# Optimization experiments

Measured on AMD Instinct MI355X. Metric: run time of the kernel, lower is better.

The kernel has to match this reference:

```python
import jax, jax.numpy as jnp
from jax import lax
import numpy as np

B, T, D, H, K = 16, 2048, 512, 512, 2

def setup_inputs() -> dict:
    key = jax.random.key(0)
    k1, k2, k3 = jax.random.split(key, 3)
    inputs = jax.random.normal(k1, (B, T, D), dtype=jnp.float32)
    conv_w = jax.random.normal(k2, (3 * H, D, K), dtype=jnp.float32) * (1.0 / np.sqrt(D * K))
    conv_b = jax.random.normal(k3, (3 * H,), dtype=jnp.float32) * 0.01
    return {"inputs": inputs, "conv_w": conv_w, "conv_b": conv_b}

def reference(inputs, conv_w, conv_b):
    # inputs: [B, T, D]; conv_w: [3H, D, K]; causal conv via left-pad K-1
    k = conv_w.shape[-1]
    h = conv_w.shape[0] // 3
    x = jnp.transpose(inputs, (0, 2, 1))                      # [B, D, T]
    x = jnp.pad(x, ((0, 0), (0, 0), (k - 1, 0)))              # left pad
    gates = lax.conv_general_dilated(
        x, conv_w, window_strides=(1,), padding='VALID',
        dimension_numbers=('NCH', 'OIH', 'NCH'))              # [B, 3H, T]
    gates = jnp.transpose(gates, (0, 2, 1)) + conv_b          # [B, T, 3H]
    Z, F, O = jnp.split(gates, 3, axis=2)
    Z = jnp.tanh(Z)
    F = jax.nn.sigmoid(F)
    O = jax.nn.sigmoid(O)

    # fo-pool: c_t = f_t * c_{t-1} + (1 - f_t) * z_t, c_{-1} = 0
    def step(c, zf):
        z, f = zf
        c_ = f * c + (1.0 - f) * z
        return c_, c_

    c0 = jnp.zeros((Z.shape[0], h), dtype=Z.dtype)
    _, C = lax.scan(step, c0, (jnp.swapaxes(Z, 0, 1), jnp.swapaxes(F, 0, 1)))
    C = jnp.swapaxes(C, 0, 1)                                 # [B, T, H]
    return C, O * C
```

## Files before the change

kernel.cpp:

```cpp
#include <hip/hip_runtime.h>


#define MTOT 32768
#define NTOT 1536
#define KTOT 1024
#define DCH  512
#define TLEN 2048
#define NB   16

#define LC2    32
#define NCH    64
#define CHAINS 8192

typedef __bf16 bf16x8 __attribute__((ext_vector_type(8)));
typedef float  f32x4  __attribute__((ext_vector_type(4)));

__device__ __forceinline__ unsigned short f2bf(float x) {
    unsigned u = __float_as_uint(x);
    u += 0x7FFFu + ((u >> 16) & 1u);
    return (unsigned short)(u >> 16);
}
__device__ __forceinline__ float bf2f(unsigned short h) {
    return __uint_as_float(((unsigned)h) << 16);
}
__device__ __forceinline__ float sigmoidf_(float x) {
    return 1.f / (1.f + __expf(-x));
}

__global__ __launch_bounds__(256) void make_A(const float* __restrict__ in,
                                              unsigned short* __restrict__ A) {
    size_t i = (size_t)blockIdx.x * 256 + threadIdx.x;
    size_t e = i * 8;
    size_t m = e >> 10;
    int    j = (int)(e & 1023);
    alignas(16) unsigned short h[8];
    if (((m & (TLEN - 1)) == 0) && (j < DCH)) {
#pragma unroll
        for (int r = 0; r < 8; ++r) h[r] = 0;
    } else {
        const float* src = in + ((long long)m - 1) * DCH + j;
        float4 a = *(const float4*)src;
        float4 b = *(const float4*)(src + 4);
        h[0] = f2bf(a.x); h[1] = f2bf(a.y); h[2] = f2bf(a.z); h[3] = f2bf(a.w);
        h[4] = f2bf(b.x); h[5] = f2bf(b.y); h[6] = f2bf(b.z); h[7] = f2bf(b.w);
    }
    *(int4*)(A + e) = *(const int4*)h;
}

__global__ __launch_bounds__(256) void make_B(const float* __restrict__ w,
                                              unsigned short* __restrict__ Bt) {
    int i = blockIdx.x * 256 + threadIdx.x;
    int o = i >> 9, d = i & 511;
    float w0 = w[(size_t)(o * 512 + d) * 2];
    float w1 = w[(size_t)(o * 512 + d) * 2 + 1];
    Bt[(size_t)o * 1024 + d]       = f2bf(w0);
    Bt[(size_t)o * 1024 + 512 + d] = f2bf(w1);
}

__global__ __launch_bounds__(512) void gemm_gates(const unsigned short* __restrict__ A,
                                                  const unsigned short* __restrict__ B,
                                                  const float* __restrict__ bias,
                                                  unsigned short* __restrict__ GT) {
    __shared__ int4 lds4[8192];

    const int tid = threadIdx.x;
    const int bx0 = blockIdx.x;
    const int bx  = (bx0 & 7) * 96 + (bx0 >> 3);
    const int mT  = bx / 6, nT = bx % 6;
    const int m0  = mT * 256, n0 = nT * 256;

    const int sq = (tid & 3) ^ ((tid >> 3) & 3);
    const unsigned short* ga = A + (size_t)(m0 + (tid >> 2)) * 1024 + sq * 8;
    const unsigned short* gb = B + (size_t)(n0 + (tid >> 2)) * 1024 + sq * 8;
    char* ldsc = (char*)lds4;

    const int lane = tid & 63;
    const int wv   = tid >> 6;
    const int wm   = wv >> 2, wn = wv & 3;
    const int lr   = lane & 15, lq = lane >> 4;

    int aoff[2][4], boff[4];
#pragma unroll
    for (int ih = 0; ih < 2; ++ih)
#pragma unroll
        for (int i = 0; i < 4; ++i) {
            int r = wm * 128 + ih * 64 + i * 16 + lr;
            aoff[ih][i] = r * 4 + (lq ^ ((r >> 1) & 3));
        }
#pragma unroll
    for (int j = 0; j < 4; ++j) {
        int c = wn * 64 + j * 16 + lr;
        boff[j] = 1024 + c * 4 + (lq ^ ((c >> 1) & 3));
    }

    f32x4 acc[8][4] = {};
    bf16x8 bfr[4];

#define GLL(SRC, DOFF) __builtin_amdgcn_global_load_lds( \
        (__attribute__((address_space(1))) void*)(void*)(SRC), \
        (__attribute__((address_space(3))) void*)(ldsc + (DOFF)), 16, 0, 0)

#define STG_A(S, KH) { const size_t go_ = (size_t)(S) * 64 + (size_t)(KH) * 32; \
        const int db_ = ((((S) & 1) * 4096 + (KH) * 2048) * 16) + tid * 16; \
        GLL(ga + go_, db_); GLL(ga + 131072 + go_, db_ + 8192); }
#define STG_B(S, KH) { const size_t go_ = (size_t)(S) * 64 + (size_t)(KH) * 32; \
        const int db_ = ((((S) & 1) * 4096 + (KH) * 2048) * 16) + 16384 + tid * 16; \
        GLL(gb + go_, db_); GLL(gb + 131072 + go_, db_ + 8192); }

#define VMW(N) asm volatile("s_waitcnt vmcnt(" #N ")" ::: "memory")

#define PHASE(D, KH, IH, RDB, STG, VM) { \
        const int rg_ = (D) * 4096 + (KH) * 2048; \
        if (RDB) { \
            _Pragma("unroll") \
            for (int j = 0; j < 4; ++j) bfr[j] = __builtin_bit_cast(bf16x8, lds4[rg_ + boff[j]]); \
        } \
        bf16x8 af_[4]; \
        _Pragma("unroll") \
        for (int i = 0; i < 4; ++i) af_[i] = __builtin_bit_cast(bf16x8, lds4[rg_ + aoff[IH][i]]); \
        STG; \
        __builtin_amdgcn_sched_barrier(0); \
        __builtin_amdgcn_s_barrier(); \
        __builtin_amdgcn_sched_barrier(0); \
        __builtin_amdgcn_s_setprio(1); \
        _Pragma("unroll") \
        for (int i = 0; i < 4; ++i) \
            _Pragma("unroll") \
            for (int j = 0; j < 4; ++j) \
                acc[(IH) * 4 + i][j] = __builtin_amdgcn_mfma_f32_16x16x32_bf16( \
                    af_[i], bfr[j], acc[(IH) * 4 + i][j], 0, 0, 0); \
        __builtin_amdgcn_s_setprio(0); \
        VM; \
        __builtin_amdgcn_sched_barrier(0); \
        __builtin_amdgcn_s_barrier(); \
        __builtin_amdgcn_sched_barrier(0); \
    }

    STG_A(0, 0); STG_B(0, 0); STG_A(0, 1); STG_B(0, 1); STG_A(1, 0); STG_B(1, 0);
    VMW(8);
    __builtin_amdgcn_s_barrier();
    __builtin_amdgcn_sched_barrier(0);

    for (int t = 0; t < 14; t += 2) {
        PHASE(0, 0, 0, 1, STG_A(t + 1, 1), ((void)0));
        PHASE(0, 0, 1, 0, STG_B(t + 1, 1), VMW(8));
        PHASE(0, 1, 0, 1, STG_A(t + 2, 0), ((void)0));
        PHASE(0, 1, 1, 0, STG_B(t + 2, 0), VMW(8));
        PHASE(1, 0, 0, 1, STG_A(t + 2, 1), ((void)0));
        PHASE(1, 0, 1, 0, STG_B(t + 2, 1), VMW(8));
        PHASE(1, 1, 0, 1, STG_A(t + 3, 0), ((void)0));
        PHASE(1, 1, 1, 0, STG_B(t + 3, 0), VMW(8));
    }
    PHASE(0, 0, 0, 1, STG_A(15, 1), ((void)0));
    PHASE(0, 0, 1, 0, STG_B(15, 1), VMW(8));
    PHASE(0, 1, 0, 1, ((void)0),    ((void)0));
    PHASE(0, 1, 1, 0, ((void)0),    VMW(4));
    PHASE(1, 0, 0, 1, ((void)0),    ((void)0));
    PHASE(1, 0, 1, 0, ((void)0),    VMW(0));
    PHASE(1, 1, 0, 1, ((void)0),    ((void)0));
    PHASE(1, 1, 1, 0, ((void)0),    ((void)0));

#undef PHASE
#undef VMW
#undef STG_A
#undef STG_B
#undef GLL

#pragma unroll
    for (int j = 0; j < 4; ++j) {
        int gn = n0 + wn * 64 + j * 16 + lr;
        float bj = bias[gn];
#pragma unroll
        for (int i = 0; i < 8; ++i) {
            int gm = m0 + wm * 128 + i * 16 + lq * 4;
            alignas(8) unsigned short pk[4];
#pragma unroll
            for (int r = 0; r < 4; ++r) pk[r] = f2bf(acc[i][j][r] + bj);
            *(int2*)(GT + (size_t)gn * MTOT + gm) = *(const int2*)pk;
        }
    }
}

__global__ __launch_bounds__(256) void scan_part1(const unsigned short* __restrict__ GT,
                                                  float* __restrict__ Pws,
                                                  float* __restrict__ Cws) {
    const int tid   = threadIdx.x;
    const int h_loc = tid & 31;
    const int sc    = tid >> 5;
    const int bid   = blockIdx.x;
    const int tg    = bid & 7;
    const int hg    = (bid >> 3) & 15;
    const int b     = bid >> 7;
    const int h     = hg * 32 + h_loc;
    const int cg    = tg * 8 + sc;

    const size_t mbase = (size_t)b * TLEN + (size_t)cg * LC2;
    const unsigned short* gz = GT + (size_t)h * MTOT + mbase;
    const unsigned short* gf = GT + (size_t)(DCH + h) * MTOT + mbase;

    bf16x8 zv[4], fv[4];
#pragma unroll
    for (int q = 0; q < 4; ++q) zv[q] = *(const bf16x8*)(gz + q * 8);
#pragma unroll
    for (int q = 0; q < 4; ++q) fv[q] = *(const bf16x8*)(gf + q * 8);

    float P = 1.f, c = 0.f;
#pragma unroll
    for (int q = 0; q < 4; ++q)
#pragma unroll
        for (int r = 0; r < 8; ++r) {
            float f = sigmoidf_((float)fv[q][r]);
            float z = 2.f * sigmoidf_(2.f * (float)zv[q][r]) - 1.f;
            c = f * c + (1.f - f) * z;
            P *= f;
        }
    const int ch = b * DCH + h;
    Pws[(size_t)cg * CHAINS + ch] = P;
    Cws[(size_t)cg * CHAINS + ch] = c;
}

__global__ __launch_bounds__(256) void scan_part2(const float* __restrict__ Pws,
                                                  const float* __restrict__ Cws,
                                                  float* __restrict__ Iws) {
    const int ch = blockIdx.x * 256 + threadIdx.x;
    float cc = 0.f;
    for (int blk = 0; blk < NCH / 16; ++blk) {
        float Pv[16], Cv[16];
#pragma unroll
        for (int i = 0; i < 16; ++i) Pv[i] = Pws[(size_t)(blk * 16 + i) * CHAINS + ch];
#pragma unroll
        for (int i = 0; i < 16; ++i) Cv[i] = Cws[(size_t)(blk * 16 + i) * CHAINS + ch];
#pragma unroll
        for (int i = 0; i < 16; ++i) {
            Iws[(size_t)(blk * 16 + i) * CHAINS + ch] = cc;
            cc = Pv[i] * cc + Cv[i];
        }
    }
}

__global__ __launch_bounds__(256) void scan_part3(const unsigned short* __restrict__ GT,
                                                  const float* __restrict__ Iws,
                                                  float* __restrict__ out) {
    const int tid   = threadIdx.x;
    const int h_loc = tid & 31;
    const int sc    = tid >> 5;
    const int bid   = blockIdx.x;
    const int tg    = bid & 7;
    const int hg    = (bid >> 3) & 15;
    const int b     = bid >> 7;
    const int h     = hg * 32 + h_loc;
    const int cg    = tg * 8 + sc;

    const size_t mbase = (size_t)b * TLEN + (size_t)cg * LC2;
    const unsigned short* gz = GT + (size_t)h * MTOT + mbase;
    const unsigned short* gf = GT + (size_t)(DCH + h) * MTOT + mbase;
    const unsigned short* go = GT + (size_t)(2 * DCH + h) * MTOT + mbase;

    bf16x8 zv[4], fv[4], ov[4];
#pragma unroll
    for (int q = 0; q < 4; ++q) zv[q] = *(const bf16x8*)(gz + q * 8);
#pragma unroll
    for (int q = 0; q < 4; ++q) fv[q] = *(const bf16x8*)(gf + q * 8);
#pragma unroll
    for (int q = 0; q < 4; ++q) ov[q] = *(const bf16x8*)(go + q * 8);

    const int ch = b * DCH + h;
    float c = Iws[(size_t)cg * CHAINS + ch];

    const size_t BTH = (size_t)NB * TLEN * DCH;
    float* oC  = out + mbase * DCH + h;
    float* oOC = oC + BTH;
#pragma unroll
    for (int q = 0; q < 4; ++q)
#pragma unroll
        for (int r = 0; r < 8; ++r) {
            float f = sigmoidf_((float)fv[q][r]);
            float z = 2.f * sigmoidf_(2.f * (float)zv[q][r]) - 1.f;
            float o = sigmoidf_((float)ov[q][r]);
            c = f * c + (1.f - f) * z;
            __builtin_nontemporal_store(c,     oC  + (size_t)(q * 8 + r) * DCH);
            __builtin_nontemporal_store(o * c, oOC + (size_t)(q * 8 + r) * DCH);
        }
}

extern "C" void kernel_launch(void* const* d_in, const int* in_sizes, int n_in,
                              void* d_out, int out_size, void* d_ws, size_t ws_size,
                              hipStream_t stream) {
    const float* in   = (const float*)d_in[0];
    const float* w    = (const float*)d_in[1];
    const float* bias = (const float*)d_in[2];
    float* out = (float*)d_out;

    unsigned short* Abf = (unsigned short*)d_ws;
    unsigned short* Bbf = Abf + (size_t)MTOT * 1024;
    unsigned short* GT  = Bbf + (size_t)NTOT * 1024;

    float* Pws = (float*)d_ws;
    float* Cws = Pws + (size_t)NCH * CHAINS;
    float* Iws = Cws + (size_t)NCH * CHAINS;

    make_A<<<dim3(16384), dim3(256), 0, stream>>>(in, Abf);
    make_B<<<dim3(3072),  dim3(256), 0, stream>>>(w, Bbf);
    gemm_gates<<<dim3(768), dim3(512), 0, stream>>>(Abf, Bbf, bias, GT);
    scan_part1<<<dim3(2048), dim3(256), 0, stream>>>(GT, Pws, Cws);
    scan_part2<<<dim3(CHAINS / 256), dim3(256), 0, stream>>>(Pws, Cws, Iws);
    scan_part3<<<dim3(2048), dim3(256), 0, stream>>>(GT, Iws, out);
}
```

Before: 361.5 us.

## Merge A/B prep kernels and cut GEMM phase barriers to one per phase

Combines the input-to-bf16 conversion kernel and the weight-transpose kernel into one launch that dispatches on block index, removing one launch and its inter-kernel gap. In the GEMM main loop, each phase now issues its vmcnt wait and a single barrier before the MFMAs, instead of a barrier both before and after. This halves the workgroup barriers per phase. It also adds waits to phases that had none, which may expose global-load latency and could introduce an LDS hazard if the double-buffer reasoning does not hold.

```diff
diff --git a/kernel.cpp b/kernel.cpp
--- a/kernel.cpp
+++ b/kernel.cpp
@@ -20,41 +20,40 @@
     u += 0x7FFFu + ((u >> 16) & 1u);
     return (unsigned short)(u >> 16);
 }
-__device__ __forceinline__ float bf2f(unsigned short h) {
-    return __uint_as_float(((unsigned)h) << 16);
-}
 __device__ __forceinline__ float sigmoidf_(float x) {
     return 1.f / (1.f + __expf(-x));
 }
 
-__global__ __launch_bounds__(256) void make_A(const float* __restrict__ in,
-                                              unsigned short* __restrict__ A) {
-    size_t i = (size_t)blockIdx.x * 256 + threadIdx.x;
-    size_t e = i * 8;
-    size_t m = e >> 10;
-    int    j = (int)(e & 1023);
-    alignas(16) unsigned short h[8];
-    if (((m & (TLEN - 1)) == 0) && (j < DCH)) {
-#pragma unroll
-        for (int r = 0; r < 8; ++r) h[r] = 0;
+__global__ __launch_bounds__(256) void make_AB(const float* __restrict__ in,
+                                               const float* __restrict__ w,
+                                               unsigned short* __restrict__ A,
+                                               unsigned short* __restrict__ Bt) {
+    const int bx = blockIdx.x;
+    if (bx < 16384) {
+        size_t i = (size_t)bx * 256 + threadIdx.x;
+        size_t e = i * 8;
+        size_t m = e >> 10;
+        int    j = (int)(e & 1023);
+        alignas(16) unsigned short h[8];
+        if (((m & (TLEN - 1)) == 0) && (j < DCH)) {
+#pragma unroll
+            for (int r = 0; r < 8; ++r) h[r] = 0;
+        } else {
+            const float* src = in + ((long long)m - 1) * DCH + j;
+            float4 a = *(const float4*)src;
+            float4 b = *(const float4*)(src + 4);
+            h[0] = f2bf(a.x); h[1] = f2bf(a.y); h[2] = f2bf(a.z); h[3] = f2bf(a.w);
+            h[4] = f2bf(b.x); h[5] = f2bf(b.y); h[6] = f2bf(b.z); h[7] = f2bf(b.w);
+        }
+        *(int4*)(A + e) = *(const int4*)h;
     } else {
-        const float* src = in + ((long long)m - 1) * DCH + j;
-        float4 a = *(const float4*)src;
-        float4 b = *(const float4*)(src + 4);
-        h[0] = f2bf(a.x); h[1] = f2bf(a.y); h[2] = f2bf(a.z); h[3] = f2bf(a.w);
-        h[4] = f2bf(b.x); h[5] = f2bf(b.y); h[6] = f2bf(b.z); h[7] = f2bf(b.w);
-    }
-    *(int4*)(A + e) = *(const int4*)h;
-}
-
-__global__ __launch_bounds__(256) void make_B(const float* __restrict__ w,
-                                              unsigned short* __restrict__ Bt) {
-    int i = blockIdx.x * 256 + threadIdx.x;
-    int o = i >> 9, d = i & 511;
-    float w0 = w[(size_t)(o * 512 + d) * 2];
-    float w1 = w[(size_t)(o * 512 + d) * 2 + 1];
-    Bt[(size_t)o * 1024 + d]       = f2bf(w0);
-    Bt[(size_t)o * 1024 + 512 + d] = f2bf(w1);
+        int i = (bx - 16384) * 256 + threadIdx.x;
+        int o = i >> 9, d = i & 511;
+        float w0 = w[(size_t)(o * 512 + d) * 2];
+        float w1 = w[(size_t)(o * 512 + d) * 2 + 1];
+        Bt[(size_t)o * 1024 + d]       = f2bf(w0);
+        Bt[(size_t)o * 1024 + 512 + d] = f2bf(w1);
+    }
 }
 
 __global__ __launch_bounds__(512) void gemm_gates(const unsigned short* __restrict__ A,
@@ -119,6 +118,7 @@
         _Pragma("unroll") \
         for (int i = 0; i < 4; ++i) af_[i] = __builtin_bit_cast(bf16x8, lds4[rg_ + aoff[IH][i]]); \
         STG; \
+        VM; \
         __builtin_amdgcn_sched_barrier(0); \
         __builtin_amdgcn_s_barrier(); \
         __builtin_amdgcn_sched_barrier(0); \
@@ -130,32 +130,29 @@
                 acc[(IH) * 4 + i][j] = __builtin_amdgcn_mfma_f32_16x16x32_bf16( \
                     af_[i], bfr[j], acc[(IH) * 4 + i][j], 0, 0, 0); \
         __builtin_amdgcn_s_setprio(0); \
-        VM; \
-        __builtin_amdgcn_sched_barrier(0); \
-        __builtin_amdgcn_s_barrier(); \
-        __builtin_amdgcn_sched_barrier(0); \
     }
 
     STG_A(0, 0); STG_B(0, 0); STG_A(0, 1); STG_B(0, 1); STG_A(1, 0); STG_B(1, 0);
     VMW(8);
+    __builtin_amdgcn_sched_barrier(0);
     __builtin_amdgcn_s_barrier();
     __builtin_amdgcn_sched_barrier(0);
 
     for (int t = 0; t < 14; t += 2) {
-        PHASE(0, 0, 0, 1, STG_A(t + 1, 1), ((void)0));
+        PHASE(0, 0, 0, 1, STG_A(t + 1, 1), VMW(8));
         PHASE(0, 0, 1, 0, STG_B(t + 1, 1), VMW(8));
-        PHASE(0, 1, 0, 1, STG_A(t + 2, 0), ((void)0));
+        PHASE(0, 1, 0, 1, STG_A(t + 2, 0), VMW(8));
         PHASE(0, 1, 1, 0, STG_B(t + 2, 0), VMW(8));
-        PHASE(1, 0, 0, 1, STG_A(t + 2, 1), ((void)0));
+        PHASE(1, 0, 0, 1, STG_A(t + 2, 1), VMW(8));
         PHASE(1, 0, 1, 0, STG_B(t + 2, 1), VMW(8));
-        PHASE(1, 1, 0, 1, STG_A(t + 3, 0), ((void)0));
+        PHASE(1, 1, 0, 1, STG_A(t + 3, 0), VMW(8));
         PHASE(1, 1, 1, 0, STG_B(t + 3, 0), VMW(8));
     }
-    PHASE(0, 0, 0, 1, STG_A(15, 1), ((void)0));
+    PHASE(0, 0, 0, 1, STG_A(15, 1), VMW(8));
     PHASE(0, 0, 1, 0, STG_B(15, 1), VMW(8));
-    PHASE(0, 1, 0, 1, ((void)0),    ((void)0));
+    PHASE(0, 1, 0, 1, ((void)0),    VMW(4));
     PHASE(0, 1, 1, 0, ((void)0),    VMW(4));
-    PHASE(1, 0, 0, 1, ((void)0),    ((void)0));
+    PHASE(1, 0, 0, 1, ((void)0),    VMW(0));
     PHASE(1, 0, 1, 0, ((void)0),    VMW(0));
     PHASE(1, 1, 0, 1, ((void)0),    ((void)0));
     PHASE(1, 1, 1, 0, ((void)0),    ((void)0));
@@ -299,8 +296,7 @@
     float* Cws = Pws + (size_t)NCH * CHAINS;
     float* Iws = Cws + (size_t)NCH * CHAINS;
 
-    make_A<<<dim3(16384), dim3(256), 0, stream>>>(in, Abf);
-    make_B<<<dim3(3072),  dim3(256), 0, stream>>>(w, Bbf);
+    make_AB<<<dim3(19456), dim3(256), 0, stream>>>(in, w, Abf, Bbf);
     gemm_gates<<<dim3(768), dim3(512), 0, stream>>>(Abf, Bbf, bias, GT);
     scan_part1<<<dim3(2048), dim3(256), 0, stream>>>(GT, Pws, Cws);
     scan_part2<<<dim3(CHAINS / 256), dim3(256), 0, stream>>>(Pws, Cws, Iws);
```

New measurement: 362.6 us. No clear change (+0.3%).
